# Performance work log

Hardware: AMD Instinct MI355X
Metric: run time of the kernel (lower is better)

The kernel has to match this reference:

```python
import jax, jax.numpy as jnp
import numpy as np

D_MODEL = 1024
H = 16
D_FF = 2048
EPS = 1e-5


def _ln(x, g, b):
    m = jnp.mean(x, axis=-1, keepdims=True)
    v = jnp.mean((x - m) ** 2, axis=-1, keepdims=True)
    return (x - m) * jax.lax.rsqrt(v + EPS) * g + b


def setup_inputs() -> dict:
    key = jax.random.key(0)
    ks = jax.random.split(key, 16)
    d, dff = D_MODEL, D_FF
    s = 1.0 / np.sqrt(d)
    inp = {
        "x": jax.random.normal(ks[0], (2, 2048, d), jnp.float32),
        "Wq": jax.random.normal(ks[1], (d, d), jnp.float32) * s,
        "bq": jax.random.normal(ks[2], (d,), jnp.float32) * 0.01,
        "Wk": jax.random.normal(ks[3], (d, d), jnp.float32) * s,
        "bk": jax.random.normal(ks[4], (d,), jnp.float32) * 0.01,
        "Wv": jax.random.normal(ks[5], (d, d), jnp.float32) * s,
        "bv": jax.random.normal(ks[6], (d,), jnp.float32) * 0.01,
        "Wo": jax.random.normal(ks[7], (d, d), jnp.float32) * s,
        "bo": jax.random.normal(ks[8], (d,), jnp.float32) * 0.01,
        "ln1_g": 1.0 + 0.1 * jax.random.normal(ks[9], (d,), jnp.float32),
        "ln1_b": 0.01 * jax.random.normal(ks[10], (d,), jnp.float32),
        "ln2_g": 1.0 + 0.1 * jax.random.normal(ks[11], (d,), jnp.float32),
        "ln2_b": 0.01 * jax.random.normal(ks[12], (d,), jnp.float32),
        "W1": jax.random.normal(ks[13], (d, dff), jnp.float32) * s,
        "b1": 0.01 * jax.random.normal(ks[14], (dff,), jnp.float32),
        "W2": jax.random.normal(ks[15], (dff, d), jnp.float32) * (1.0 / np.sqrt(dff)),
        "b2": jnp.zeros((d,), jnp.float32),
    }
    return inp


def reference(x, Wq, bq, Wk, bk, Wv, bv, Wo, bo, ln1_g, ln1_b, ln2_g, ln2_b, W1, b1, W2, b2):
    b, s, d = x.shape
    dk = d // H

    # --- sublayer 1: pre-LN self-attention with residual (dropout = eval/identity) ---
    y = _ln(x, ln1_g, ln1_b)
    q = (y @ Wq + bq).reshape(b, s, H, dk).transpose(0, 2, 1, 3)  # (b,h,s,dk)
    k = (y @ Wk + bk).reshape(b, s, H, dk).transpose(0, 2, 1, 3)
    v = (y @ Wv + bv).reshape(b, s, H, dk).transpose(0, 2, 1, 3)
    scores = jnp.einsum("bhqd,bhkd->bhqk", q, k) / jnp.sqrt(jnp.float32(dk))
    attn = jax.nn.softmax(scores, axis=-1)
    o = jnp.einsum("bhqk,bhkd->bhqd", attn, v)  # (b,h,s,dk)
    # faithful to original bug: transpose last two dims then flat reshape
    o = jnp.swapaxes(o, -1, -2).reshape(b, s, d)  # (b,h,dk,s) -> (b,s,d)
    x = x + (o @ Wo + bo)

    # --- sublayer 2: pre-LN FFN with residual ---
    y2 = _ln(x, ln2_g, ln2_b)
    f = jax.nn.relu(y2 @ W1 + b1) @ W2 + b2
    return x + f
```

## Files before the change

### kernel.cpp

```cpp
#include <hip/hip_runtime.h>
#include <hip/hip_bf16.h>

#define D_MODEL 1024
#define NHEAD 16
#define DK 64
#define DFF 2048
#define SEQ 2048
#define NBATCH 2
#define NTOK (NBATCH*SEQ)

typedef __attribute__((ext_vector_type(8))) short bf16x8;
typedef __attribute__((ext_vector_type(4))) float f32x4;
typedef __attribute__((ext_vector_type(16))) float f32x16;
typedef __attribute__((ext_vector_type(4))) short s16x4;

#if __has_builtin(__builtin_amdgcn_exp2f)
#define EXP2(x) __builtin_amdgcn_exp2f(x)
#else
#define EXP2(x) exp2f(x)
#endif

__device__ __forceinline__ short f2bf(float f) {
    union { float f; unsigned u; } v; v.f = f;
    unsigned r = v.u + 0x7FFFu + ((v.u >> 16) & 1u);
    return (short)(r >> 16);
}

__device__ __forceinline__ void gld16(void* lds, const void* g) {
    __builtin_amdgcn_global_load_lds(
        (const __attribute__((address_space(1))) void*)g,
        (__attribute__((address_space(3))) void*)lds, 16, 0, 0);
}

__global__ __launch_bounds__(256) void k_transpose(const float* __restrict__ W,
                                                   short* __restrict__ WT, int K, int N)
{
    __shared__ float t[32][33];
    int tid = threadIdx.x;
    int n0 = blockIdx.x * 32, k0 = blockIdx.y * 32;
#pragma unroll
    for (int p = 0; p < 4; ++p) {
        int idx = p * 256 + tid, r = idx >> 5, c = idx & 31;
        t[r][c] = W[(size_t)(k0 + r) * N + (n0 + c)];
    }
    __syncthreads();
#pragma unroll
    for (int p = 0; p < 4; ++p) {
        int idx = p * 256 + tid, r = idx >> 5, c = idx & 31;
        WT[(size_t)(n0 + r) * K + (k0 + c)] = f2bf(t[c][r]);
    }
}

struct TP4 { const float* src[4]; short* dst[4]; };
__global__ __launch_bounds__(256) void k_transpose4(TP4 tp)
{
    __shared__ float t[32][33];
    const float* W = tp.src[blockIdx.z];
    short* WT = tp.dst[blockIdx.z];
    const int K = 1024, N = 1024;
    int tid = threadIdx.x;
    int n0 = blockIdx.x * 32, k0 = blockIdx.y * 32;
#pragma unroll
    for (int p = 0; p < 4; ++p) {
        int idx = p * 256 + tid, r = idx >> 5, c = idx & 31;
        t[r][c] = W[(size_t)(k0 + r) * N + (n0 + c)];
    }
    __syncthreads();
#pragma unroll
    for (int p = 0; p < 4; ++p) {
        int idx = p * 256 + tid, r = idx >> 5, c = idx & 31;
        WT[(size_t)(n0 + r) * K + (k0 + c)] = f2bf(t[c][r]);
    }
}

__global__ __launch_bounds__(256) void k_layernorm(const float* __restrict__ x,
                                                   const float* __restrict__ g,
                                                   const float* __restrict__ bta,
                                                   short* __restrict__ y)
{
    int row = blockIdx.x * 4 + (threadIdx.x >> 6);
    int lane = threadIdx.x & 63;
    const float* xr = x + (size_t)row * D_MODEL;
    float4 v[4];
    float s = 0.f, s2 = 0.f;
#pragma unroll
    for (int c = 0; c < 4; ++c) {
        v[c] = *(const float4*)(xr + c * 256 + lane * 4);
        s  += v[c].x + v[c].y + v[c].z + v[c].w;
        s2 += v[c].x * v[c].x + v[c].y * v[c].y + v[c].z * v[c].z + v[c].w * v[c].w;
    }
#pragma unroll
    for (int off = 1; off < 64; off <<= 1) {
        s  += __shfl_xor(s, off, 64);
        s2 += __shfl_xor(s2, off, 64);
    }
    float mean = s * (1.f / 1024.f);
    float var  = s2 * (1.f / 1024.f) - mean * mean;
    float rs = rsqrtf(var + 1e-5f);
    short* yr = y + (size_t)row * D_MODEL;
#pragma unroll
    for (int c = 0; c < 4; ++c) {
        int idx = c * 256 + lane * 4;
        float4 gg = *(const float4*)(g + idx);
        float4 bb = *(const float4*)(bta + idx);
        s16x4 o;
        o.x = f2bf((v[c].x - mean) * rs * gg.x + bb.x);
        o.y = f2bf((v[c].y - mean) * rs * gg.y + bb.y);
        o.z = f2bf((v[c].z - mean) * rs * gg.z + bb.z);
        o.w = f2bf((v[c].w - mean) * rs * gg.w + bb.w);
        *(s16x4*)(yr + idx) = o;
    }
}

template<int EPI, int BN>
__global__ __launch_bounds__(256) void k_gemm(
    const short* __restrict__ A, const short* __restrict__ BT, int N, int K,
    const float* __restrict__ bias, const float* __restrict__ bias2, const float* __restrict__ bias3,
    const float* __restrict__ resid, float* __restrict__ outF,
    short* __restrict__ outB, short* __restrict__ outQ, short* __restrict__ outK, short* __restrict__ outV)
{
    constexpr int NJ = BN / 32;
    __shared__ __align__(16) short sA[3][128 * 32];
    __shared__ __align__(16) short sB[3][BN * 32];
    int tid = threadIdx.x;
    int lane = tid & 63, wid = tid >> 6;
    int wr = wid >> 1, wc = wid & 1;
    int lrow = lane & 15, lk8 = (lane >> 4) * 8;

    int gx = gridDim.x;
    int nwg = gx * gridDim.y;
    int orig = blockIdx.x + blockIdx.y * gx;
    int wg = (orig & 7) * (nwg >> 3) + (orig >> 3);
    int bx = wg % gx, by = wg / gx;

    const short* Ab = A + (size_t)by * 128 * K;
    const short* Bb = BT + (size_t)bx * BN * K;

    int cA0 = tid, cA1 = 256 + tid;
    const char* pA0 = (const char*)(Ab + (size_t)(cA0 >> 2) * K + (cA0 & 3) * 8);
    const char* pA1 = (const char*)(Ab + (size_t)(cA1 >> 2) * K + (cA1 & 3) * 8);
    const char* pB0 = (const char*)(Bb + (size_t)(cA0 >> 2) * K + (cA0 & 3) * 8);
    const char* pB1 = (const char*)(Bb + (size_t)(cA1 >> 2) * K + (cA1 & 3) * 8);

    auto stage = [&](int buf) {
        gld16(&sA[buf][cA0 * 8], pA0);  pA0 += 64;
        gld16(&sA[buf][cA1 * 8], pA1);  pA1 += 64;
        if constexpr (BN == 128) {
            gld16(&sB[buf][cA0 * 8], pB0);  pB0 += 64;
            gld16(&sB[buf][cA1 * 8], pB1);  pB1 += 64;
        } else {
            gld16(&sB[buf][cA0 * 8], pB0);  pB0 += 64;
        }
    };

    const f32x4 fz = {0.f, 0.f, 0.f, 0.f};
    f32x4 acc[4][NJ];
#pragma unroll
    for (int i = 0; i < 4; i++)
#pragma unroll
        for (int j = 0; j < NJ; j++) acc[i][j] = fz;

    const int NT = K / 32;
    stage(0);
    stage(1);
    int cur = 0;
    for (int t = 0; t < NT; ++t) {
        if (t + 2 < NT) {
            int nb3 = cur + 2; if (nb3 >= 3) nb3 -= 3;
            stage(nb3);
            if constexpr (BN == 128) asm volatile("s_waitcnt vmcnt(8)" ::: "memory");
            else                     asm volatile("s_waitcnt vmcnt(6)" ::: "memory");
        } else if (t + 1 < NT) {
            if constexpr (BN == 128) asm volatile("s_waitcnt vmcnt(4)" ::: "memory");
            else                     asm volatile("s_waitcnt vmcnt(3)" ::: "memory");
        } else {
            asm volatile("s_waitcnt vmcnt(0)" ::: "memory");
        }
        __builtin_amdgcn_s_barrier();
        bf16x8 af[4], bfr[NJ];
#pragma unroll
        for (int i = 0; i < 4; i++) af[i]  = *(const bf16x8*)&sA[cur][(wr * 64 + i * 16 + lrow) * 32 + lk8];
#pragma unroll
        for (int j = 0; j < NJ; j++) bfr[j] = *(const bf16x8*)&sB[cur][(wc * (BN/2) + j * 16 + lrow) * 32 + lk8];
#pragma unroll
        for (int i = 0; i < 4; i++)
#pragma unroll
            for (int j = 0; j < NJ; j++)
                acc[i][j] = __builtin_amdgcn_mfma_f32_16x16x32_bf16(af[i], bfr[j], acc[i][j], 0, 0, 0);
        __builtin_amdgcn_s_barrier();
        ++cur; if (cur >= 3) cur = 0;
    }

    int m_base = by * 128 + wr * 64 + (lane >> 4) * 4;
    int n_base = bx * BN + wc * (BN/2) + lrow;
#pragma unroll
    for (int i = 0; i < 4; i++) {
#pragma unroll
        for (int j = 0; j < NJ; j++) {
            int n = n_base + j * 16;
#pragma unroll
            for (int jj = 0; jj < 4; jj++) {
                int m = m_base + i * 16 + jj;
                float v = acc[i][j][jj];
                if constexpr (EPI == 0) {
                    int seg = n >> 10, nn = n & 1023;
                    int b = m >> 11, ss = m & 2047;
                    int h = nn >> 6, dd = nn & 63;
                    if (seg == 0) {
                        outQ[(((size_t)(b * NHEAD + h)) * SEQ + ss) * DK + dd] =
                            f2bf((v + bias[nn]) * 0.18033688011112042f);
                    } else if (seg == 1) {
                        outK[(((size_t)(b * NHEAD + h)) * SEQ + ss) * DK + dd] = f2bf(v + bias2[nn]);
                    } else {
                        outV[(((size_t)(b * NHEAD + h)) * DK + dd) * SEQ + ss] = f2bf(v + bias3[nn]);
                    }
                } else if constexpr (EPI == 1) {
                    size_t idx = (size_t)m * N + n;
                    outF[idx] = v + bias[n] + resid[idx];
                } else if constexpr (EPI == 2) {
                    float r2 = v + bias[n];
                    outB[(size_t)m * N + n] = f2bf(r2 > 0.f ? r2 : 0.f);
                } else {
                    size_t idx = (size_t)m * N + n;
                    outF[idx] = v + bias[n] + resid[idx];
                }
            }
        }
    }
}

__global__ __launch_bounds__(256) void k_attn(const short* __restrict__ Q, const short* __restrict__ Kk,
                                              const short* __restrict__ Vt, short* __restrict__ Operm)
{
    __shared__ __align__(16) short sMem[2][2][64 * 64];
    int tid = threadIdx.x, lane = tid & 63;
    int wid = tid >> 6;
    int qg = wid >> 1, ks = wid & 1;
    int l31 = lane & 31, hi = lane >> 5;

    int orig = blockIdx.x + blockIdx.y * 32;
    int lg = (orig & 7) * 128 + (orig >> 3);
    int bh = lg >> 5, qt = lg & 31;
    int b = bh >> 4, h = bh & 15;
    int q0 = qt * 64 + qg * 32;
    const short* Qp = Q + (size_t)bh * SEQ * DK;
    const short* Kp = Kk + (size_t)bh * SEQ * DK;
    const short* Vp = Vt + (size_t)bh * DK * SEQ;

    bf16x8 qf[4];
#pragma unroll
    for (int kb = 0; kb < 4; ++kb)
        qf[kb] = *(const bf16x8*)(Qp + (size_t)(q0 + l31) * DK + kb * 16 + hi * 8);

    int c0 = tid, c1 = 256 + tid;
    int r0 = c0 >> 3, r1 = c1 >> 3;
    const char* pK0 = (const char*)(Kp + (size_t)r0 * DK) + (((c0 & 7) ^ (r0 & 7)) << 4);
    const char* pK1 = (const char*)(Kp + (size_t)r1 * DK) + (((c1 & 7) ^ (r1 & 7)) << 4);
    const char* pV0 = (const char*)(Vp + (size_t)r0 * SEQ) + (((c0 & 7) ^ (r0 & 7)) << 4);
    const char* pV1 = (const char*)(Vp + (size_t)r1 * SEQ) + (((c1 & 7) ^ (r1 & 7)) << 4);

    auto stage = [&](int buf) {
        gld16(&sMem[buf][0][c0 * 8], pK0);  pK0 += 8192;
        gld16(&sMem[buf][0][c1 * 8], pK1);  pK1 += 8192;
        gld16(&sMem[buf][1][c0 * 8], pV0);  pV0 += 128;
        gld16(&sMem[buf][1][c1 * 8], pV1);  pV1 += 128;
    };

    f32x16 Oa0 = {0,0,0,0,0,0,0,0,0,0,0,0,0,0,0,0};
    f32x16 Oa1 = {0,0,0,0,0,0,0,0,0,0,0,0,0,0,0,0};
    float lsum = 0.f;

    stage(0);
    const int NT = SEQ / 64;
    int krow = ks * 32 + l31;
    int sw = (l31 & 7) << 4;
    for (int t = 0; t < NT; ++t) {
        int cur = t & 1;
        if (t + 1 < NT) {
            stage(cur ^ 1);
            asm volatile("s_waitcnt vmcnt(4)" ::: "memory");
        } else {
            asm volatile("s_waitcnt vmcnt(0)" ::: "memory");
        }
        __builtin_amdgcn_s_barrier();
        const char* sKc = (const char*)sMem[cur][0];
        const char* sVc = (const char*)sMem[cur][1];

        f32x16 sc = {0,0,0,0,0,0,0,0,0,0,0,0,0,0,0,0};
#pragma unroll
        for (int kb = 0; kb < 4; ++kb) {
            int cb = (kb * 32 + hi * 16) ^ sw;
            bf16x8 kf = *(const bf16x8*)(sKc + krow * 128 + cb);
            sc = __builtin_amdgcn_mfma_f32_32x32x16_bf16(kf, qf[kb], sc, 0, 0, 0);
        }

        unsigned W[4][2];
#pragma unroll
        for (int tt = 0; tt < 4; ++tt) {
            float pa_ = EXP2(sc[4*tt+0]), pb_ = EXP2(sc[4*tt+1]);
            float pc_ = EXP2(sc[4*tt+2]), pd_ = EXP2(sc[4*tt+3]);
            lsum += (pa_ + pb_) + (pc_ + pd_);
            asm("v_cvt_pk_bf16_f32 %0, %1, %2" : "=v"(W[tt][0]) : "v"(pa_), "v"(pb_));
            asm("v_cvt_pk_bf16_f32 %0, %1, %2" : "=v"(W[tt][1]) : "v"(pc_), "v"(pd_));
        }

        auto pv_step = [&](unsigned a0, unsigned a1, unsigned b0v, unsigned b1v, int kslice) {
            asm("v_permlane32_swap_b32 %0, %1" : "+v"(a0), "+v"(b0v));
            asm("v_permlane32_swap_b32 %0, %1" : "+v"(a1), "+v"(b1v));
            union { unsigned u[4]; bf16x8 v; } pa;
            pa.u[0] = a0; pa.u[1] = a1; pa.u[2] = b0v; pa.u[3] = b1v;
            int cb = (kslice * 32 + hi * 16) ^ sw;
            bf16x8 vf0 = *(const bf16x8*)(sVc + l31 * 128 + cb);
            bf16x8 vf1 = *(const bf16x8*)(sVc + (32 + l31) * 128 + cb);
            Oa0 = __builtin_amdgcn_mfma_f32_32x32x16_bf16(pa.v, vf0, Oa0, 0, 0, 0);
            Oa1 = __builtin_amdgcn_mfma_f32_32x32x16_bf16(pa.v, vf1, Oa1, 0, 0, 0);
        };
        pv_step(W[0][0], W[0][1], W[1][0], W[1][1], ks * 2 + 0);
        pv_step(W[2][0], W[2][1], W[3][0], W[3][1], ks * 2 + 1);
        __builtin_amdgcn_s_barrier();
    }

    lsum += __shfl_xor(lsum, 32, 64);

    float* mrg = (float*)sMem;
    if (ks == 1) {
        float* m0 = mrg + (qg * 64 + lane) * 33;
#pragma unroll
        for (int i = 0; i < 16; ++i) m0[i] = Oa0[i];
#pragma unroll
        for (int i = 0; i < 16; ++i) m0[16 + i] = Oa1[i];
        m0[32] = lsum;
    }
    __syncthreads();
    if (ks == 0) {
        const float* m0 = mrg + (qg * 64 + lane) * 33;
#pragma unroll
        for (int i = 0; i < 16; ++i) Oa0[i] += m0[i];
#pragma unroll
        for (int i = 0; i < 16; ++i) Oa1[i] += m0[16 + i];
        lsum += m0[32];

        float rlv[16];
#pragma unroll
        for (int tt = 0; tt < 4; ++tt)
#pragma unroll
            for (int rr = 0; rr < 4; ++rr) {
                float ts = __shfl(lsum, 4 * hi + 8 * tt + rr, 64);
                rlv[4 * tt + rr] = 1.f / ts;
            }

        int qcol = (q0 & 1023) + 4 * hi;
        int qhi = q0 >> 10;
#pragma unroll
        for (int db = 0; db < 2; ++db) {
            const f32x16& O = db ? Oa1 : Oa0;
            int dd = db * 32 + l31;
            size_t rowoff = ((size_t)b * SEQ + h * 128 + 2 * dd + qhi) * D_MODEL + qcol;
#pragma unroll
            for (int tt = 0; tt < 4; ++tt) {
                s16x4 o;
                o.x = f2bf(O[4*tt+0] * rlv[4*tt+0]);
                o.y = f2bf(O[4*tt+1] * rlv[4*tt+1]);
                o.z = f2bf(O[4*tt+2] * rlv[4*tt+2]);
                o.w = f2bf(O[4*tt+3] * rlv[4*tt+3]);
                *(s16x4*)(Operm + rowoff + 8 * tt) = o;
            }
        }
    }
}

extern "C" void kernel_launch(void* const* d_in, const int* in_sizes, int n_in,
                              void* d_out, int out_size, void* d_ws, size_t ws_size,
                              hipStream_t stream)
{
    const float* x   = (const float*)d_in[0];
    const float* Wq  = (const float*)d_in[1];
    const float* bq  = (const float*)d_in[2];
    const float* Wk  = (const float*)d_in[3];
    const float* bk  = (const float*)d_in[4];
    const float* Wv  = (const float*)d_in[5];
    const float* bv  = (const float*)d_in[6];
    const float* Wo  = (const float*)d_in[7];
    const float* bo  = (const float*)d_in[8];
    const float* g1  = (const float*)d_in[9];
    const float* b1l = (const float*)d_in[10];
    const float* g2  = (const float*)d_in[11];
    const float* b2l = (const float*)d_in[12];
    const float* W1  = (const float*)d_in[13];
    const float* b1  = (const float*)d_in[14];
    const float* W2  = (const float*)d_in[15];
    const float* b2  = (const float*)d_in[16];
    float* out = (float*)d_out;

    char* ws = (char*)d_ws;
    size_t off = 0;
    auto alloc = [&](size_t bytes) {
        char* p = ws + off;
        off += (bytes + 255) & ~(size_t)255;
        return p;
    };
    short* WqkvT = (short*)alloc((size_t)3072 * 1024 * 2);
    short* WoT   = (short*)alloc((size_t)1024 * 1024 * 2);
    short* W1T   = (short*)alloc((size_t)2048 * 1024 * 2);
    short* W2T   = (short*)alloc((size_t)1024 * 2048 * 2);
    short* Y     = (short*)alloc((size_t)NTOK * 1024 * 2);
    short* Qb    = (short*)alloc((size_t)NTOK * 1024 * 2);
    short* Kb    = (short*)alloc((size_t)NTOK * 1024 * 2);
    short* Vtb   = (short*)alloc((size_t)NTOK * 1024 * 2);
    short* Operm = (short*)alloc((size_t)NTOK * 1024 * 2);
    float* X1    = (float*)alloc((size_t)NTOK * 1024 * 4);
    short* F1    = (short*)alloc((size_t)NTOK * 2048 * 2);

    TP4 tp;
    tp.src[0] = Wq; tp.dst[0] = WqkvT;
    tp.src[1] = Wk; tp.dst[1] = WqkvT + 1024 * 1024;
    tp.src[2] = Wv; tp.dst[2] = WqkvT + 2048 * 1024;
    tp.src[3] = Wo; tp.dst[3] = WoT;
    k_transpose4<<<dim3(32, 32, 4), 256, 0, stream>>>(tp);
    k_transpose<<<dim3(64, 32), 256, 0, stream>>>(W1, W1T, 1024, 2048);
    k_transpose<<<dim3(32, 64), 256, 0, stream>>>(W2, W2T, 2048, 1024);

    k_layernorm<<<NTOK / 4, 256, 0, stream>>>(x, g1, b1l, Y);

    k_gemm<0,128><<<dim3(24, 32), 256, 0, stream>>>(Y, WqkvT, 3072, 1024,
        bq, bk, bv, nullptr, nullptr, nullptr, Qb, Kb, Vtb);

    k_attn<<<dim3(32, 32), 256, 0, stream>>>(Qb, Kb, Vtb, Operm);

    k_gemm<1,64><<<dim3(16, 32), 256, 0, stream>>>(Operm, WoT, 1024, 1024,
        bo, nullptr, nullptr, x, X1, nullptr, nullptr, nullptr, nullptr);

    k_layernorm<<<NTOK / 4, 256, 0, stream>>>(X1, g2, b2l, Y);

    k_gemm<2,128><<<dim3(16, 32), 256, 0, stream>>>(Y, W1T, 2048, 1024,
        b1, nullptr, nullptr, nullptr, nullptr, F1, nullptr, nullptr, nullptr);

    k_gemm<3,64><<<dim3(16, 32), 256, 0, stream>>>(F1, W2T, 1024, 2048,
        b2, nullptr, nullptr, X1, out, nullptr, nullptr, nullptr, nullptr);
}
```

Baseline: 206.3 us.

## XOR-swizzle GEMM LDS tiles and use 8-wave blocks for 128-wide tiles

Applies an XOR swizzle to the 16-byte chunks of each 32-element K row in shared memory, on both the global-to-LDS copy and the fragment reads, to cut LDS bank conflicts. The BN=128 GEMMs (QKV and FFN1) now run with 512 threads, so each wave computes a 64x32 subtile and each thread issues one load per operand per stage. More waves per block adds latency hiding, but each wave gets less reuse and the barrier involves more waves. Wait counts are adjusted to match.

```diff
diff --git a/kernel.cpp b/kernel.cpp
--- a/kernel.cpp
+++ b/kernel.cpp
@@ -112,20 +112,21 @@
     }
 }
 
-template<int EPI, int BN>
-__global__ __launch_bounds__(256) void k_gemm(
+template<int EPI, int BN, int THREADS>
+__global__ __launch_bounds__(THREADS) void k_gemm(
     const short* __restrict__ A, const short* __restrict__ BT, int N, int K,
     const float* __restrict__ bias, const float* __restrict__ bias2, const float* __restrict__ bias3,
     const float* __restrict__ resid, float* __restrict__ outF,
     short* __restrict__ outB, short* __restrict__ outQ, short* __restrict__ outK, short* __restrict__ outV)
 {
-    constexpr int NJ = BN / 32;
+    constexpr int CW = THREADS / 128;
     __shared__ __align__(16) short sA[3][128 * 32];
     __shared__ __align__(16) short sB[3][BN * 32];
     int tid = threadIdx.x;
     int lane = tid & 63, wid = tid >> 6;
-    int wr = wid >> 1, wc = wid & 1;
-    int lrow = lane & 15, lk8 = (lane >> 4) * 8;
+    int wr = wid / CW, wc = wid % CW;
+    int lrow = lane & 15;
+    int lk16 = (lane >> 4) << 4;
 
     int gx = gridDim.x;
     int nwg = gx * gridDim.y;
@@ -136,29 +137,33 @@
     const short* Ab = A + (size_t)by * 128 * K;
     const short* Bb = BT + (size_t)bx * BN * K;
 
-    int cA0 = tid, cA1 = 256 + tid;
-    const char* pA0 = (const char*)(Ab + (size_t)(cA0 >> 2) * K + (cA0 & 3) * 8);
-    const char* pA1 = (const char*)(Ab + (size_t)(cA1 >> 2) * K + (cA1 & 3) * 8);
-    const char* pB0 = (const char*)(Bb + (size_t)(cA0 >> 2) * K + (cA0 & 3) * 8);
-    const char* pB1 = (const char*)(Bb + (size_t)(cA1 >> 2) * K + (cA1 & 3) * 8);
+    auto src = [&](const short* base, int cc) {
+        int r = cc >> 2, s = cc & 3;
+        return (const char*)(base + (size_t)r * K) + (((s ^ ((r >> 1) & 3)) << 4));
+    };
+    const char *pA0, *pA1 = nullptr, *pB0;
+    pA0 = src(Ab, tid);
+    pB0 = src(Bb, tid & (BN * 4 - 1));
+    if constexpr (THREADS == 256) pA1 = src(Ab, 256 + tid);
 
     auto stage = [&](int buf) {
-        gld16(&sA[buf][cA0 * 8], pA0);  pA0 += 64;
-        gld16(&sA[buf][cA1 * 8], pA1);  pA1 += 64;
-        if constexpr (BN == 128) {
-            gld16(&sB[buf][cA0 * 8], pB0);  pB0 += 64;
-            gld16(&sB[buf][cA1 * 8], pB1);  pB1 += 64;
+        if constexpr (THREADS == 512) {
+            gld16(&sA[buf][tid * 8], pA0);  pA0 += 64;
+            gld16(&sB[buf][tid * 8], pB0);  pB0 += 64;
         } else {
-            gld16(&sB[buf][cA0 * 8], pB0);  pB0 += 64;
+            gld16(&sA[buf][tid * 8], pA0);          pA0 += 64;
+            gld16(&sA[buf][(256 + tid) * 8], pA1);  pA1 += 64;
+            gld16(&sB[buf][(tid & (BN * 4 - 1)) * 8], pB0);  pB0 += 64;
         }
     };
+    constexpr int LPS = (THREADS == 512) ? 2 : 3;
 
     const f32x4 fz = {0.f, 0.f, 0.f, 0.f};
-    f32x4 acc[4][NJ];
+    f32x4 acc[4][2];
 #pragma unroll
     for (int i = 0; i < 4; i++)
 #pragma unroll
-        for (int j = 0; j < NJ; j++) acc[i][j] = fz;
+        for (int j = 0; j < 2; j++) acc[i][j] = fz;
 
     const int NT = K / 32;
     stage(0);
@@ -168,35 +173,41 @@
         if (t + 2 < NT) {
             int nb3 = cur + 2; if (nb3 >= 3) nb3 -= 3;
             stage(nb3);
-            if constexpr (BN == 128) asm volatile("s_waitcnt vmcnt(8)" ::: "memory");
-            else                     asm volatile("s_waitcnt vmcnt(6)" ::: "memory");
+            if constexpr (LPS == 2) asm volatile("s_waitcnt vmcnt(4)" ::: "memory");
+            else                    asm volatile("s_waitcnt vmcnt(6)" ::: "memory");
         } else if (t + 1 < NT) {
-            if constexpr (BN == 128) asm volatile("s_waitcnt vmcnt(4)" ::: "memory");
-            else                     asm volatile("s_waitcnt vmcnt(3)" ::: "memory");
+            if constexpr (LPS == 2) asm volatile("s_waitcnt vmcnt(2)" ::: "memory");
+            else                    asm volatile("s_waitcnt vmcnt(3)" ::: "memory");
         } else {
             asm volatile("s_waitcnt vmcnt(0)" ::: "memory");
         }
         __builtin_amdgcn_s_barrier();
-        bf16x8 af[4], bfr[NJ];
-#pragma unroll
-        for (int i = 0; i < 4; i++) af[i]  = *(const bf16x8*)&sA[cur][(wr * 64 + i * 16 + lrow) * 32 + lk8];
-#pragma unroll
-        for (int j = 0; j < NJ; j++) bfr[j] = *(const bf16x8*)&sB[cur][(wc * (BN/2) + j * 16 + lrow) * 32 + lk8];
+        bf16x8 af[4], bfr[2];
+#pragma unroll
+        for (int i = 0; i < 4; i++) {
+            int row = wr * 64 + i * 16 + lrow;
+            af[i] = *(const bf16x8*)((const char*)sA[cur] + row * 64 + (lk16 ^ (((row >> 1) & 3) << 4)));
+        }
+#pragma unroll
+        for (int j = 0; j < 2; j++) {
+            int row = wc * 32 + j * 16 + lrow;
+            bfr[j] = *(const bf16x8*)((const char*)sB[cur] + row * 64 + (lk16 ^ (((row >> 1) & 3) << 4)));
+        }
 #pragma unroll
         for (int i = 0; i < 4; i++)
 #pragma unroll
-            for (int j = 0; j < NJ; j++)
+            for (int j = 0; j < 2; j++)
                 acc[i][j] = __builtin_amdgcn_mfma_f32_16x16x32_bf16(af[i], bfr[j], acc[i][j], 0, 0, 0);
         __builtin_amdgcn_s_barrier();
         ++cur; if (cur >= 3) cur = 0;
     }
 
     int m_base = by * 128 + wr * 64 + (lane >> 4) * 4;
-    int n_base = bx * BN + wc * (BN/2) + lrow;
+    int n_base = bx * BN + wc * 32 + lrow;
 #pragma unroll
     for (int i = 0; i < 4; i++) {
 #pragma unroll
-        for (int j = 0; j < NJ; j++) {
+        for (int j = 0; j < 2; j++) {
             int n = n_base + j * 16;
 #pragma unroll
             for (int jj = 0; jj < 4; jj++) {
@@ -422,19 +433,19 @@
 
     k_layernorm<<<NTOK / 4, 256, 0, stream>>>(x, g1, b1l, Y);
 
-    k_gemm<0,128><<<dim3(24, 32), 256, 0, stream>>>(Y, WqkvT, 3072, 1024,
+    k_gemm<0,128,512><<<dim3(24, 32), 512, 0, stream>>>(Y, WqkvT, 3072, 1024,
         bq, bk, bv, nullptr, nullptr, nullptr, Qb, Kb, Vtb);
 
     k_attn<<<dim3(32, 32), 256, 0, stream>>>(Qb, Kb, Vtb, Operm);
 
-    k_gemm<1,64><<<dim3(16, 32), 256, 0, stream>>>(Operm, WoT, 1024, 1024,
+    k_gemm<1,64,256><<<dim3(16, 32), 256, 0, stream>>>(Operm, WoT, 1024, 1024,
         bo, nullptr, nullptr, x, X1, nullptr, nullptr, nullptr, nullptr);
 
     k_layernorm<<<NTOK / 4, 256, 0, stream>>>(X1, g2, b2l, Y);
 
-    k_gemm<2,128><<<dim3(16, 32), 256, 0, stream>>>(Y, W1T, 2048, 1024,
+    k_gemm<2,128,512><<<dim3(16, 32), 512, 0, stream>>>(Y, W1T, 2048, 1024,
         b1, nullptr, nullptr, nullptr, nullptr, F1, nullptr, nullptr, nullptr);
 
-    k_gemm<3,64><<<dim3(16, 32), 256, 0, stream>>>(F1, W2T, 1024, 2048,
+    k_gemm<3,64,256><<<dim3(16, 32), 256, 0, stream>>>(F1, W2T, 1024, 2048,
         b2, nullptr, nullptr, X1, out, nullptr, nullptr, nullptr, nullptr);
 }
```

Measured after the change: 199.1 us. 3.5% less time.
